# Performance work log

Measured on AMD Instinct MI355X. Metric: run time of the kernel, lower is better.

## Reference

```python
import jax, jax.numpy as jnp
import numpy as np
from jax import lax

H = 64          # lstm_units per direction
FEAT = 128      # input feature dim
EMB = 128       # dense output dim (embedding_dim)
B, T = 512, 512


def setup_inputs() -> dict:
    key = jax.random.key(0)
    ks = jax.random.split(key, 9)
    s = 0.05
    return {
        "x": jax.random.normal(ks[0], (B, T, FEAT), dtype=jnp.float32),
        # Keras LSTM kernels: input kernel [F, 4H], recurrent kernel [H, 4H], bias [4H]
        # gate order: i, f, g(cell), o
        "W_fwd": jax.random.normal(ks[1], (FEAT, 4 * H), dtype=jnp.float32) * s,
        "U_fwd": jax.random.normal(ks[2], (H, 4 * H), dtype=jnp.float32) * s,
        "b_fwd": jnp.zeros((4 * H,), dtype=jnp.float32),
        "W_bwd": jax.random.normal(ks[3], (FEAT, 4 * H), dtype=jnp.float32) * s,
        "U_bwd": jax.random.normal(ks[4], (H, 4 * H), dtype=jnp.float32) * s,
        "b_bwd": jnp.zeros((4 * H,), dtype=jnp.float32),
        "W_dense": jax.random.normal(ks[5], (2 * H, EMB), dtype=jnp.float32) * s,
        "b_dense": jnp.zeros((EMB,), dtype=jnp.float32),
    }


def _lstm_last(x, W, U, b):
    """Run an LSTM over x [B,T,F]; return last hidden state [B,H]."""
    bsz = x.shape[0]
    # precompute input projections for all timesteps (one big GEMM)
    xp = jnp.einsum('btf,fg->btg', x, W) + b      # [B,T,4H]
    xp = jnp.swapaxes(xp, 0, 1)                   # [T,B,4H]
    h0 = jnp.zeros((bsz, H), x.dtype)
    c0 = jnp.zeros((bsz, H), x.dtype)

    def step(carry, xt):
        h, c = carry
        z = xt + h @ U                            # [B,4H]
        i = jax.nn.sigmoid(z[:, :H])
        f = jax.nn.sigmoid(z[:, H:2 * H])
        g = jnp.tanh(z[:, 2 * H:3 * H])
        o = jax.nn.sigmoid(z[:, 3 * H:])
        c = f * c + i * g
        h = o * jnp.tanh(c)
        return (h, c), None

    (h, _), _ = lax.scan(step, (h0, c0), xp)
    return h


def reference(x, W_fwd, U_fwd, b_fwd, W_bwd, U_bwd, b_bwd, W_dense, b_dense):
    # Bidirectional(LSTM(return_sequences=False)), merge_mode='concat'.
    # dropout=0.2 is inactive at inference (training=False), so no dropout here.
    h_f = _lstm_last(x, W_fwd, U_fwd, b_fwd)
    h_b = _lstm_last(x[:, ::-1, :], W_bwd, U_bwd, b_bwd)
    h = jnp.concatenate([h_f, h_b], axis=-1)      # [B, 2H]
    return jax.nn.relu(h @ W_dense + b_dense)     # [B, EMB]
```

## Files before the change

kernel.cpp:

```cpp
#include <hip/hip_runtime.h>
#include <hip/hip_bf16.h>

#define H 64
#define F 128
#define G4 256
#define T 512
#define B 512
#define RB 16
#define TC 8

typedef __attribute__((ext_vector_type(4))) float f32x4;
typedef __attribute__((ext_vector_type(8))) short bf16x8;

__device__ __forceinline__ short f2bf(float f) {
    union { float f; unsigned u; } v; v.f = f;
    unsigned r = (v.u + 0x7fffu + ((v.u >> 16) & 1u)) >> 16;
    return (short)r;
}
__device__ __forceinline__ short f2bf_cvt(float f) {
    unsigned r;
    asm("v_cvt_pk_bf16_f32 %0, %1, %1" : "=v"(r) : "v"(f));
    return (short)r;
}
__device__ __forceinline__ unsigned cvtpk(float lo, float hi) {
    unsigned r;
    asm("v_cvt_pk_bf16_f32 %0, %1, %2" : "=v"(r) : "v"(lo), "v"(hi));
    return r;
}
__device__ __forceinline__ float bf2f(short s) {
    union { unsigned u; float f; } v; v.u = ((unsigned)(unsigned short)s) << 16;
    return v.f;
}
__device__ __forceinline__ float bflo(unsigned u) {
    union { unsigned u; float f; } v; v.u = u << 16; return v.f;
}
__device__ __forceinline__ float bfhi(unsigned u) {
    union { unsigned u; float f; } v; v.u = u & 0xffff0000u; return v.f;
}
__device__ __forceinline__ float sigf(float x) {
    return __builtin_amdgcn_rcpf(1.f + __expf(-x));
}
__device__ __forceinline__ float tanhf_(float x) {
    float e = __expf(2.f * x);
    return 1.f - 2.f * __builtin_amdgcn_rcpf(e + 1.f);
}

#define LOADX(XR, TT) do {                                                     \
    int _b = (TT) * F + 4 * lq;                                                \
    _Pragma("unroll")                                                          \
    for (int kt = 0; kt < 4; ++kt) {                                           \
        XR[kt][0] = *(const f32x4*)(xlane + _b + 32 * kt);                     \
        XR[kt][1] = *(const f32x4*)(xlane + _b + 32 * kt + 16);                \
    }                                                                          \
} while (0)

#define STOREXP(DIRBASE, SLOT, ACC) do {                                       \
    size_t _base = ((size_t)((DIRBASE) + rowg * 4 + lq) * (T / 2)              \
                    + ((SLOT) >> 1)) * 4096                                    \
                   + ((SLOT) & 1) * 512 + (16 * w + lr) * 8;                   \
    _Pragma("unroll")                                                          \
    for (int e = 0; e < 4; ++e) {                                              \
        uint2 pv;                                                              \
        pv.x = cvtpk(ACC[0][e], ACC[1][e]);                                    \
        pv.y = cvtpk(ACC[2][e], ACC[3][e]);                                    \
        *(uint2*)(xpb + _base + e * 1024) = pv;                                \
    }                                                                          \
} while (0)

#define XBODY2(TCUR, XR) do {                                                  \
    bf16x8 af[4];                                                              \
    _Pragma("unroll")                                                          \
    for (int kt = 0; kt < 4; ++kt) {                                           \
        bf16x8 v;                                                              \
        _Pragma("unroll")                                                      \
        for (int e = 0; e < 4; ++e) {                                          \
            v[e]     = f2bf(XR[kt][0][e]);                                     \
            v[e + 4] = f2bf(XR[kt][1][e]);                                     \
        }                                                                      \
        af[kt] = v;                                                            \
    }                                                                          \
    {   int tn = (TCUR) + 2; if (tn > T - 1) tn = T - 1;                       \
        LOADX(XR, tn); }                                                       \
    {   f32x4 accf[4];                                                         \
        _Pragma("unroll")                                                      \
        for (int s = 0; s < 4; ++s)                                            \
            accf[s] = (f32x4){bscf[s], bscf[s], bscf[s], bscf[s]};             \
        _Pragma("unroll")                                                      \
        for (int kt = 0; kt < 4; ++kt)                                         \
            _Pragma("unroll")                                                  \
            for (int s = 0; s < 4; ++s)                                        \
                accf[s] = __builtin_amdgcn_mfma_f32_16x16x32_bf16(             \
                    af[kt], wff[kt][s], accf[s], 0, 0, 0);                     \
        STOREXP(0, (TCUR), accf);                                              \
    }                                                                          \
    {   f32x4 accb[4];                                                         \
        _Pragma("unroll")                                                      \
        for (int s = 0; s < 4; ++s)                                            \
            accb[s] = (f32x4){bscb[s], bscb[s], bscb[s], bscb[s]};             \
        _Pragma("unroll")                                                      \
        for (int kt = 0; kt < 4; ++kt)                                         \
            _Pragma("unroll")                                                  \
            for (int s = 0; s < 4; ++s)                                        \
                accb[s] = __builtin_amdgcn_mfma_f32_16x16x32_bf16(             \
                    af[kt], wfb[kt][s], accb[s], 0, 0, 0);                     \
        STOREXP(128, T - 1 - (TCUR), accb);                                    \
    }                                                                          \
} while (0)

__global__ __launch_bounds__(256, 1)
void xw_gemm(const float* __restrict__ x,
             const float* __restrict__ Wf, const float* __restrict__ bfv,
             const float* __restrict__ Wb, const float* __restrict__ bbv,
             char* __restrict__ xpb) {
    const int tid = threadIdx.x;
    const int l = tid & 63, w = tid >> 6;
    const int lq = l >> 4, lr = l & 15;
    const int rowg = blockIdx.x >> 3;
    const int tc   = blockIdx.x & 7;
    const int r0 = rowg * RB;
    const int t0 = tc * (T / TC);

    bf16x8 wff[4][4], wfb[4][4];
#pragma unroll
    for (int kt = 0; kt < 4; ++kt)
#pragma unroll
        for (int s = 0; s < 4; ++s) {
            int col = (w + 4 * s) * 16 + lr;
            int k0 = kt * 32 + 4 * lq;
            bf16x8 vf, vb;
#pragma unroll
            for (int e = 0; e < 4; ++e) {
                vf[e]     = f2bf(Wf[(k0 + e) * G4 + col]);
                vf[e + 4] = f2bf(Wf[(k0 + 16 + e) * G4 + col]);
                vb[e]     = f2bf(Wb[(k0 + e) * G4 + col]);
                vb[e + 4] = f2bf(Wb[(k0 + 16 + e) * G4 + col]);
            }
            wff[kt][s] = vf;
            wfb[kt][s] = vb;
        }
    float bscf[4], bscb[4];
#pragma unroll
    for (int s = 0; s < 4; ++s) {
        bscf[s] = bfv[(w + 4 * s) * 16 + lr];
        bscb[s] = bbv[(w + 4 * s) * 16 + lr];
    }

    const float* xlane = x + (size_t)(r0 + lr) * (T * F);

    f32x4 xrA[4][2], xrB[4][2];
    LOADX(xrA, t0);
    LOADX(xrB, t0 + 1);

    for (int t = t0; t < t0 + T / TC; t += 2) {
        XBODY2(t,     xrA);
        XBODY2(t + 1, xrB);
    }
}

#define STAGE(PAIR, BUF) do {                                                  \
    int _p = (PAIR); if (_p > T / 2 - 1) _p = T / 2 - 1;                       \
    const char* _g = (const char*)xpc + ((size_t)_p * 4 + w) * 1024 + 16 * l;  \
    char* _lb = xps + (BUF) * 4096 + w * 1024;                                 \
    __builtin_amdgcn_global_load_lds(                                          \
        (const __attribute__((address_space(1))) void*)_g,                     \
        (__attribute__((address_space(3))) void*)_lb, 16, 0, 0);               \
} while (0)

#define RSTEP(TCUR, BUF, PRD, PWR, DOSTAGE) do {                               \
    bf16x8 hf0 = *(const bf16x8*)(hlds + (PRD) * 2048 + rd_off);               \
    bf16x8 hf1 = *(const bf16x8*)(hlds + (PRD) * 2048 + 1024 + rd_off);        \
    f32x4 acc[4];                                                              \
    _Pragma("unroll")                                                          \
    for (int s = 0; s < 4; ++s) acc[s] = (f32x4){0.f, 0.f, 0.f, 0.f};          \
    _Pragma("unroll")                                                          \
    for (int s = 0; s < 4; ++s)                                                \
        acc[s] = __builtin_amdgcn_mfma_f32_16x16x32_bf16(                      \
            hf0, ufr[0][s], acc[s], 0, 0, 0);                                  \
    _Pragma("unroll")                                                          \
    for (int s = 0; s < 4; ++s)                                                \
        acc[s] = __builtin_amdgcn_mfma_f32_16x16x32_bf16(                      \
            hf1, ufr[1][s], acc[s], 0, 0, 0);                                  \
    if (lq == 0) {                                                             \
        _Pragma("unroll")                                                      \
        for (int e = 0; e < 4; ++e) {                                          \
            f32x4 zw = {acc[0][e], acc[1][e], acc[2][e], acc[3][e]};           \
            *(f32x4*)(zbc + e * 1024 + w * 256 + lr * 16) = zw;                \
        }                                                                      \
    }                                                                          \
    asm volatile("s_waitcnt lgkmcnt(0)" ::: "memory");                         \
    __builtin_amdgcn_s_barrier();                                              \
    asm volatile("s_waitcnt vmcnt(3)" ::: "memory");                           \
    __builtin_amdgcn_sched_barrier(0);                                         \
    f32x4 zv = *(const f32x4*)(zbc + tid * 16);                                \
    uint2 xv = *(const uint2*)(xps + (BUF) * 4096 + w * 1024                   \
                               + ((TCUR) & 1) * 512 + l * 8);                  \
    float zi = zv[0] + bflo(xv.x);                                             \
    float zf = zv[1] + bfhi(xv.x);                                             \
    float zg = zv[2] + bflo(xv.y);                                             \
    float zo = zv[3] + bfhi(xv.y);                                             \
    float ei = __expf(-zi);                                                    \
    float ef = __expf(-zf);                                                    \
    float eg = __expf(2.f * fminf(zg, 15.f));                                  \
    float sf = __builtin_amdgcn_rcpf(1.f + ef);                                \
    float dig = __builtin_amdgcn_rcpf((1.f + ei) * (1.f + eg));                \
    cc = fmaf(sf, cc, (eg - 1.f) * dig);                                       \
    float eo = __expf(-zo);                                                    \
    float ec = __expf(2.f * fminf(cc, 15.f));                                  \
    float doc = __builtin_amdgcn_rcpf((1.f + eo) * (1.f + ec));                \
    hh = (ec - 1.f) * doc;                                                     \
    *(short*)(hlds + (PWR) * 2048 + wr) = f2bf_cvt(hh);                        \
    asm volatile("s_waitcnt lgkmcnt(0)" ::: "memory");                         \
    if (DOSTAGE) { STAGE(((TCUR) >> 1) + 4, BUF); }                            \
    __builtin_amdgcn_sched_barrier(0);                                         \
    __builtin_amdgcn_s_barrier();                                              \
    __builtin_amdgcn_sched_barrier(0);                                         \
} while (0)

__global__ __launch_bounds__(256, 1)
void lstm_rec(const char* __restrict__ xpb,
              const float* __restrict__ Uf, const float* __restrict__ Ub,
              float* __restrict__ hcat ) {
    const int tid = threadIdx.x;
    const int l = tid & 63, w = tid >> 6;
    const int lq = l >> 4, lr = l & 15;
    const int dir = blockIdx.x >> 7;
    const int rowg = blockIdx.x & 127;
    const int r0 = rowg * 4;

    const float* __restrict__ Um = dir ? Ub : Uf;

    bf16x8 ufr[2][4];
#pragma unroll
    for (int kt = 0; kt < 2; ++kt)
#pragma unroll
        for (int s = 0; s < 4; ++s) {
            int col = (w + 4 * s) * 16 + lr;
            int k0 = kt * 32 + 4 * lq;
            bf16x8 v;
#pragma unroll
            for (int e = 0; e < 4; ++e) {
                v[e]     = f2bf(Um[(k0 + e) * G4 + col]);
                v[e + 4] = f2bf(Um[(k0 + 16 + e) * G4 + col]);
            }
            ufr[kt][s] = v;
        }

    __shared__ __align__(16) char xps[4 * 4096];
    __shared__ __align__(16) char hlds[4096];
    __shared__ __align__(16) char zbc[4096];

    ((f32x4*)hlds)[tid] = (f32x4){0.f, 0.f, 0.f, 0.f};
    __syncthreads();

    const int rd_off = (l * 16) ^ (((l >> 4) & 3) << 4);

    const int gj = l;
    int wr;
    {
        int fl = w + 16 * ((gj >> 2) & 3);
        wr = (gj >> 5) * 1024 + ((fl * 16) ^ (((fl >> 4) & 3) << 4))
             + ((gj & 3) + 4 * ((gj >> 4) & 1)) * 2;
    }

    const char* xpc = xpb + (size_t)(dir * 128 + rowg) * (T / 2) * 4096;

    STAGE(0, 0);
    STAGE(1, 1);
    STAGE(2, 2);
    STAGE(3, 3);

    float cc = 0.f, hh = 0.f;

    for (int t = 0; t < T; t += 8) {
        RSTEP(t + 0, 0, 0, 1, 0);
        RSTEP(t + 1, 0, 1, 0, 1);
        RSTEP(t + 2, 1, 0, 1, 0);
        RSTEP(t + 3, 1, 1, 0, 1);
        RSTEP(t + 4, 2, 0, 1, 0);
        RSTEP(t + 5, 2, 1, 0, 1);
        RSTEP(t + 6, 3, 0, 1, 0);
        RSTEP(t + 7, 3, 1, 0, 1);
    }

    hcat[(size_t)(r0 + w) * (2 * H) + dir * H + l] = hh;
}

#define BODY(TCUR, XR, PRD, PWR) do {                                          \
    bf16x8 af[4];                                                              \
    _Pragma("unroll")                                                          \
    for (int kt = 0; kt < 4; ++kt) {                                           \
        bf16x8 v;                                                              \
        _Pragma("unroll")                                                      \
        for (int e = 0; e < 4; ++e) {                                          \
            v[e]     = f2bf(XR[kt][0][e]);                                     \
            v[e + 4] = f2bf(XR[kt][1][e]);                                     \
        }                                                                      \
        af[kt] = v;                                                            \
    }                                                                          \
    {   int tn = (TCUR) + 2; if (tn > T - 1) tn = T - 1;                       \
        int ttn = dir ? (T - 1 - tn) : tn;                                     \
        LOADX(XR, ttn); }                                                      \
    bf16x8 hf0 = *(const bf16x8*)(hlds + (PRD) * 2048 + rd_off);               \
    bf16x8 hf1 = *(const bf16x8*)(hlds + (PRD) * 2048 + 1024 + rd_off);        \
    f32x4 acc[4];                                                              \
    _Pragma("unroll")                                                          \
    for (int s = 0; s < 4; ++s)                                                \
        acc[s] = (f32x4){bsc[s], bsc[s], bsc[s], bsc[s]};                      \
    _Pragma("unroll")                                                          \
    for (int kt = 0; kt < 4; ++kt)                                             \
        _Pragma("unroll")                                                      \
        for (int s = 0; s < 4; ++s)                                            \
            acc[s] = __builtin_amdgcn_mfma_f32_16x16x32_bf16(                  \
                af[kt], wfr[kt][s], acc[s], 0, 0, 0);                          \
    _Pragma("unroll")                                                          \
    for (int s = 0; s < 4; ++s)                                                \
        acc[s] = __builtin_amdgcn_mfma_f32_16x16x32_bf16(                      \
            hf0, ufr[0][s], acc[s], 0, 0, 0);                                  \
    _Pragma("unroll")                                                          \
    for (int s = 0; s < 4; ++s)                                                \
        acc[s] = __builtin_amdgcn_mfma_f32_16x16x32_bf16(                      \
            hf1, ufr[1][s], acc[s], 0, 0, 0);                                  \
    _Pragma("unroll")                                                          \
    for (int e = 0; e < 4; ++e) {                                              \
        float ig = sigf(acc[0][e]);                                            \
        float fg = sigf(acc[1][e]);                                            \
        float gg = tanhf_(acc[2][e]);                                          \
        float og = sigf(acc[3][e]);                                            \
        c4[e] = fmaf(fg, c4[e], ig * gg);                                      \
        hq[e] = og * tanhf_(c4[e]);                                            \
        *(short*)(hlds + (PWR) * 2048 + wr_off[e]) = f2bf(hq[e]);              \
    }                                                                          \
    __syncthreads();                                                           \
} while (0)

__global__ __launch_bounds__(256, 1)
void lstm_mfma(const float* __restrict__ x,
               const float* __restrict__ Wf, const float* __restrict__ Uf,
               const float* __restrict__ bfv,
               const float* __restrict__ Wb, const float* __restrict__ Ub,
               const float* __restrict__ bbv,
               float* __restrict__ hcat) {
    const int tid = threadIdx.x;
    const int l = tid & 63, w = tid >> 6;
    const int lq = l >> 4, lr = l & 15;
    const int dir = blockIdx.x >> 5;
    const int r0 = (blockIdx.x & 31) * RB;

    const float* __restrict__ Wm = dir ? Wb : Wf;
    const float* __restrict__ Um = dir ? Ub : Uf;
    const float* __restrict__ bv = dir ? bbv : bfv;

    bf16x8 wfr[4][4];
#pragma unroll
    for (int kt = 0; kt < 4; ++kt)
#pragma unroll
        for (int s = 0; s < 4; ++s) {
            int col = (w + 4 * s) * 16 + lr;
            int k0 = kt * 32 + 4 * lq;
            bf16x8 v;
#pragma unroll
            for (int e = 0; e < 4; ++e) {
                v[e]     = f2bf(Wm[(k0 + e) * G4 + col]);
                v[e + 4] = f2bf(Wm[(k0 + 16 + e) * G4 + col]);
            }
            wfr[kt][s] = v;
        }
    bf16x8 ufr[2][4];
#pragma unroll
    for (int kt = 0; kt < 2; ++kt)
#pragma unroll
        for (int s = 0; s < 4; ++s) {
            int col = (w + 4 * s) * 16 + lr;
            int k0 = kt * 32 + 4 * lq;
            bf16x8 v;
#pragma unroll
            for (int e = 0; e < 4; ++e) {
                v[e]     = f2bf(Um[(k0 + e) * G4 + col]);
                v[e + 4] = f2bf(Um[(k0 + 16 + e) * G4 + col]);
            }
            ufr[kt][s] = v;
        }
    float bsc[4];
#pragma unroll
    for (int s = 0; s < 4; ++s) bsc[s] = bv[(w + 4 * s) * 16 + lr];

    __shared__ __align__(16) char hlds[4096];
    ((f32x4*)hlds)[tid] = (f32x4){0.f, 0.f, 0.f, 0.f};
    __syncthreads();

    const int rd_off = (l * 16) ^ (((l >> 4) & 3) << 4);
    const int j = 16 * w + lr;
    const int kt_j = j >> 5;
    const int elem_j = (j & 3) + 4 * ((j >> 4) & 1);
    int wr_off[4];
#pragma unroll
    for (int e = 0; e < 4; ++e) {
        int fl = 4 * lq + e + 16 * ((j >> 2) & 3);
        wr_off[e] = kt_j * 1024 + ((fl * 16) ^ (((fl >> 4) & 3) << 4)) + elem_j * 2;
    }

    const float* xlane = x + (size_t)(r0 + lr) * (T * F);

    f32x4 xrA[4][2], xrB[4][2];
    { int tt0 = dir ? (T - 1) : 0; LOADX(xrA, tt0); }
    { int tt1 = dir ? (T - 2) : 1; LOADX(xrB, tt1); }

    float c4[4] = {0.f, 0.f, 0.f, 0.f};
    float hq[4] = {0.f, 0.f, 0.f, 0.f};

    for (int t = 0; t < T; t += 2) {
        BODY(t,     xrA, 0, 1);
        BODY(t + 1, xrB, 1, 0);
    }

#pragma unroll
    for (int e = 0; e < 4; ++e) {
        int row = 4 * lq + e;
        hcat[(size_t)(r0 + row) * (2 * H) + dir * H + j] = hq[e];
    }
}

__global__ void dense_kernel(const float* __restrict__ hcat,
                             const float* __restrict__ Wd,
                             const float* __restrict__ bd,
                             float* __restrict__ out) {
    const int b = blockIdx.x;
    const int e = threadIdx.x;
    float acc = bd[e];
#pragma unroll
    for (int k = 0; k < 2 * H; ++k)
        acc = fmaf(hcat[b * (2 * H) + k], Wd[k * 128 + e], acc);
    out[b * 128 + e] = fmaxf(acc, 0.f);
}

extern "C" void kernel_launch(void* const* d_in, const int* in_sizes, int n_in,
                              void* d_out, int out_size, void* d_ws, size_t ws_size,
                              hipStream_t stream) {
    const float* x       = (const float*)d_in[0];
    const float* W_fwd   = (const float*)d_in[1];
    const float* U_fwd   = (const float*)d_in[2];
    const float* b_fwd   = (const float*)d_in[3];
    const float* W_bwd   = (const float*)d_in[4];
    const float* U_bwd   = (const float*)d_in[5];
    const float* b_bwd   = (const float*)d_in[6];
    const float* W_dense = (const float*)d_in[7];
    const float* b_dense = (const float*)d_in[8];
    float* out = (float*)d_out;

    const size_t XP_BYTES = (size_t)256 * (T / 2) * 4096;
    const size_t HCAT_BYTES = (size_t)B * 2 * H * 4;

    if (ws_size >= XP_BYTES + HCAT_BYTES) {
        char*  xpb  = (char*)d_ws;
        float* hcat = (float*)((char*)d_ws + XP_BYTES);

        xw_gemm<<<dim3(32 * TC), dim3(256), 0, stream>>>(
            x, W_fwd, b_fwd, W_bwd, b_bwd, xpb);
        lstm_rec<<<dim3(256), dim3(256), 0, stream>>>(
            xpb, U_fwd, U_bwd, hcat);
        dense_kernel<<<dim3(B), dim3(128), 0, stream>>>(hcat, W_dense, b_dense, out);
    } else {
        float* hcat = (float*)d_ws;
        lstm_mfma<<<dim3(2 * (B / RB)), dim3(256), 0, stream>>>(
            x, W_fwd, U_fwd, b_fwd, W_bwd, U_bwd, b_bwd, hcat);
        dense_kernel<<<dim3(B), dim3(128), 0, stream>>>(hcat, W_dense, b_dense, out);
    }
}
```

Before: 319.4 us.

## Compute LSTM gates directly from MFMA accumulators, removing z-broadcast LDS round-trip and barrier

Instead of having lane quarter 0 write MFMA results to an LDS buffer, barrier, and have every thread read back one gate quadruple, the lq==0 lanes now compute all four rows' gate nonlinearities directly from their accumulators. The precomputed x-projection layout is changed so each such lane reads its 4 rows' gate inputs as two 16-byte loads, and the final hidden-state writes follow the new ownership. This drops one barrier and an LDS write/read per timestep on the serial recurrence path. In exchange only a quarter of the lanes do the transcendental work, four times serially, which lengthens the per-step dependent math.

Measured after the change: 410.2 us. +28.5%, slower.

```diff
diff --git a/kernel.cpp b/kernel.cpp
--- a/kernel.cpp
+++ b/kernel.cpp
@@ -57,14 +57,14 @@
 #define STOREXP(DIRBASE, SLOT, ACC) do {                                       \
     size_t _base = ((size_t)((DIRBASE) + rowg * 4 + lq) * (T / 2)              \
                     + ((SLOT) >> 1)) * 4096                                    \
-                   + ((SLOT) & 1) * 512 + (16 * w + lr) * 8;                   \
-    _Pragma("unroll")                                                          \
-    for (int e = 0; e < 4; ++e) {                                              \
-        uint2 pv;                                                              \
-        pv.x = cvtpk(ACC[0][e], ACC[1][e]);                                    \
-        pv.y = cvtpk(ACC[2][e], ACC[3][e]);                                    \
-        *(uint2*)(xpb + _base + e * 1024) = pv;                                \
-    }                                                                          \
+                   + w * 1024 + ((SLOT) & 1) * 512 + lr * 32;                  \
+    uint4 p0, p1;                                                              \
+    p0.x = cvtpk(ACC[0][0], ACC[1][0]); p0.y = cvtpk(ACC[2][0], ACC[3][0]);    \
+    p0.z = cvtpk(ACC[0][1], ACC[1][1]); p0.w = cvtpk(ACC[2][1], ACC[3][1]);    \
+    p1.x = cvtpk(ACC[0][2], ACC[1][2]); p1.y = cvtpk(ACC[2][2], ACC[3][2]);    \
+    p1.z = cvtpk(ACC[0][3], ACC[1][3]); p1.w = cvtpk(ACC[2][3], ACC[3][3]);    \
+    *(uint4*)(xpb + _base) = p0;                                               \
+    *(uint4*)(xpb + _base + 16) = p1;                                          \
 } while (0)
 
 #define XBODY2(TCUR, XR) do {                                                  \
@@ -180,35 +180,34 @@
     for (int s = 0; s < 4; ++s)                                                \
         acc[s] = __builtin_amdgcn_mfma_f32_16x16x32_bf16(                      \
             hf1, ufr[1][s], acc[s], 0, 0, 0);                                  \
-    if (lq == 0) {                                                             \
-        _Pragma("unroll")                                                      \
-        for (int e = 0; e < 4; ++e) {                                          \
-            f32x4 zw = {acc[0][e], acc[1][e], acc[2][e], acc[3][e]};           \
-            *(f32x4*)(zbc + e * 1024 + w * 256 + lr * 16) = zw;                \
-        }                                                                      \
-    }                                                                          \
-    asm volatile("s_waitcnt lgkmcnt(0)" ::: "memory");                         \
-    __builtin_amdgcn_s_barrier();                                              \
     asm volatile("s_waitcnt vmcnt(3)" ::: "memory");                           \
     __builtin_amdgcn_sched_barrier(0);                                         \
-    f32x4 zv = *(const f32x4*)(zbc + tid * 16);                                \
-    uint2 xv = *(const uint2*)(xps + (BUF) * 4096 + w * 1024                   \
-                               + ((TCUR) & 1) * 512 + l * 8);                  \
-    float zi = zv[0] + bflo(xv.x);                                             \
-    float zf = zv[1] + bfhi(xv.x);                                             \
-    float zg = zv[2] + bflo(xv.y);                                             \
-    float zo = zv[3] + bfhi(xv.y);                                             \
-    float ei = __expf(-zi);                                                    \
-    float ef = __expf(-zf);                                                    \
-    float eg = __expf(2.f * fminf(zg, 15.f));                                  \
-    float sf = __builtin_amdgcn_rcpf(1.f + ef);                                \
-    float dig = __builtin_amdgcn_rcpf((1.f + ei) * (1.f + eg));                \
-    cc = fmaf(sf, cc, (eg - 1.f) * dig);                                       \
-    float eo = __expf(-zo);                                                    \
-    float ec = __expf(2.f * fminf(cc, 15.f));                                  \
-    float doc = __builtin_amdgcn_rcpf((1.f + eo) * (1.f + ec));                \
-    hh = (ec - 1.f) * doc;                                                     \
-    *(short*)(hlds + (PWR) * 2048 + wr) = f2bf_cvt(hh);                        \
+    if (lq == 0) {                                                             \
+        const char* _xb = xps + (BUF) * 4096 + w * 1024                        \
+                          + ((TCUR) & 1) * 512 + lr * 32;                      \
+        uint4 xv0 = *(const uint4*)_xb;                                        \
+        uint4 xv1 = *(const uint4*)(_xb + 16);                                 \
+        unsigned xg[8] = {xv0.x, xv0.y, xv0.z, xv0.w,                          \
+                          xv1.x, xv1.y, xv1.z, xv1.w};                         \
+        _Pragma("unroll")                                                      \
+        for (int e = 0; e < 4; ++e) {                                          \
+            float zi = acc[0][e] + bflo(xg[2 * e]);                            \
+            float zf = acc[1][e] + bfhi(xg[2 * e]);                            \
+            float zg = acc[2][e] + bflo(xg[2 * e + 1]);                        \
+            float zo = acc[3][e] + bfhi(xg[2 * e + 1]);                        \
+            float ei = __expf(-zi);                                            \
+            float ef = __expf(-zf);                                            \
+            float eg = __expf(2.f * fminf(zg, 15.f));                          \
+            float sf = __builtin_amdgcn_rcpf(1.f + ef);                        \
+            float dig = __builtin_amdgcn_rcpf((1.f + ei) * (1.f + eg));        \
+            cc[e] = fmaf(sf, cc[e], (eg - 1.f) * dig);                         \
+            float eo = __expf(-zo);                                            \
+            float ec = __expf(2.f * fminf(cc[e], 15.f));                       \
+            float doc = __builtin_amdgcn_rcpf((1.f + eo) * (1.f + ec));        \
+            hh[e] = (ec - 1.f) * doc;                                          \
+            *(short*)(hlds + (PWR) * 2048 + wr_off[e]) = f2bf_cvt(hh[e]);      \
+        }                                                                      \
+    }                                                                          \
     asm volatile("s_waitcnt lgkmcnt(0)" ::: "memory");                         \
     if (DOSTAGE) { STAGE(((TCUR) >> 1) + 4, BUF); }                            \
     __builtin_amdgcn_sched_barrier(0);                                         \
@@ -247,19 +246,22 @@
 
     __shared__ __align__(16) char xps[4 * 4096];
     __shared__ __align__(16) char hlds[4096];
-    __shared__ __align__(16) char zbc[4096];
-
-    ((f32x4*)hlds)[tid] = (f32x4){0.f, 0.f, 0.f, 0.f};
+
+    ((f32x4*)hlds)[tid & 255] = (f32x4){0.f, 0.f, 0.f, 0.f};
     __syncthreads();
 
     const int rd_off = (l * 16) ^ (((l >> 4) & 3) << 4);
 
-    const int gj = l;
-    int wr;
+    int wr_off[4];
     {
-        int fl = w + 16 * ((gj >> 2) & 3);
-        wr = (gj >> 5) * 1024 + ((fl * 16) ^ (((fl >> 4) & 3) << 4))
-             + ((gj & 3) + 4 * ((gj >> 4) & 1)) * 2;
+        int j = 16 * w + lr;
+        int elem_j = (j & 3) + 4 * ((j >> 4) & 1);
+#pragma unroll
+        for (int e = 0; e < 4; ++e) {
+            int fl = e + 16 * ((j >> 2) & 3);
+            wr_off[e] = (j >> 5) * 1024 + ((fl * 16) ^ (((fl >> 4) & 3) << 4))
+                        + elem_j * 2;
+        }
     }
 
     const char* xpc = xpb + (size_t)(dir * 128 + rowg) * (T / 2) * 4096;
@@ -269,7 +271,8 @@
     STAGE(2, 2);
     STAGE(3, 3);
 
-    float cc = 0.f, hh = 0.f;
+    float cc[4] = {0.f, 0.f, 0.f, 0.f};
+    float hh[4] = {0.f, 0.f, 0.f, 0.f};
 
     for (int t = 0; t < T; t += 8) {
         RSTEP(t + 0, 0, 0, 1, 0);
@@ -282,7 +285,11 @@
         RSTEP(t + 7, 3, 1, 0, 1);
     }
 
-    hcat[(size_t)(r0 + w) * (2 * H) + dir * H + l] = hh;
+    if (lq == 0) {
+#pragma unroll
+        for (int e = 0; e < 4; ++e)
+            hcat[(size_t)(r0 + e) * (2 * H) + dir * H + 16 * w + lr] = hh[e];
+    }
 }
 
 #define BODY(TCUR, XR, PRD, PWR) do {                                          \
```

## Halve rows per recurrent block to double grid and re-layout staged projections

Applied to the files above, without the earlier changes.

The recurrent kernel now handles 2 batch rows per block instead of 4, launching 512 blocks rather than 256. The precomputed input projections are re-laid out in quad-timestep chunks so that each 4 KB stage covers 4 timesteps for 2 rows. Only half of each wave's lanes run the gate math. This spreads the serial recurrence over more CUs to shorten the critical path. In exchange each MFMA does half-empty work, and one of the per-step barriers is removed.

New measurement: 340.5 us. +6.6%, slower.

```diff
diff --git a/kernel.cpp b/kernel.cpp
--- a/kernel.cpp
+++ b/kernel.cpp
@@ -55,15 +55,17 @@
 } while (0)
 
 #define STOREXP(DIRBASE, SLOT, ACC) do {                                       \
-    size_t _base = ((size_t)((DIRBASE) + rowg * 4 + lq) * (T / 2)              \
-                    + ((SLOT) >> 1)) * 4096                                    \
-                   + ((SLOT) & 1) * 512 + (16 * w + lr) * 8;                   \
     _Pragma("unroll")                                                          \
     for (int e = 0; e < 4; ++e) {                                              \
+        int grow = 4 * lq + e;                                                 \
+        size_t _a = ((size_t)((DIRBASE) + rowg * 8 + (grow >> 1)) * (T / 4)    \
+                     + ((SLOT) >> 2)) * 4096                                   \
+                    + w * 1024 + ((SLOT) & 3) * 256 + (grow & 1) * 128         \
+                    + lr * 8;                                                  \
         uint2 pv;                                                              \
         pv.x = cvtpk(ACC[0][e], ACC[1][e]);                                    \
         pv.y = cvtpk(ACC[2][e], ACC[3][e]);                                    \
-        *(uint2*)(xpb + _base + e * 1024) = pv;                                \
+        *(uint2*)(xpb + _a) = pv;                                              \
     }                                                                          \
 } while (0)
 
@@ -103,7 +105,7 @@
             for (int s = 0; s < 4; ++s)                                        \
                 accb[s] = __builtin_amdgcn_mfma_f32_16x16x32_bf16(             \
                     af[kt], wfb[kt][s], accb[s], 0, 0, 0);                     \
-        STOREXP(128, T - 1 - (TCUR), accb);                                    \
+        STOREXP(256, T - 1 - (TCUR), accb);                                    \
     }                                                                          \
 } while (0)
 
@@ -157,9 +159,9 @@
     }
 }
 
-#define STAGE(PAIR, BUF) do {                                                  \
-    int _p = (PAIR); if (_p > T / 2 - 1) _p = T / 2 - 1;                       \
-    const char* _g = (const char*)xpc + ((size_t)_p * 4 + w) * 1024 + 16 * l;  \
+#define STAGE(QUAD, BUF) do {                                                  \
+    int _q = (QUAD); if (_q > T / 4 - 1) _q = T / 4 - 1;                       \
+    const char* _g = (const char*)xpc + (size_t)_q * 4096 + w * 1024 + 16 * l; \
     char* _lb = xps + (BUF) * 4096 + w * 1024;                                 \
     __builtin_amdgcn_global_load_lds(                                          \
         (const __attribute__((address_space(1))) void*)_g,                     \
@@ -182,35 +184,37 @@
             hf1, ufr[1][s], acc[s], 0, 0, 0);                                  \
     if (lq == 0) {                                                             \
         _Pragma("unroll")                                                      \
-        for (int e = 0; e < 4; ++e) {                                          \
+        for (int e = 0; e < 2; ++e) {                                          \
             f32x4 zw = {acc[0][e], acc[1][e], acc[2][e], acc[3][e]};           \
             *(f32x4*)(zbc + e * 1024 + w * 256 + lr * 16) = zw;                \
         }                                                                      \
     }                                                                          \
     asm volatile("s_waitcnt lgkmcnt(0)" ::: "memory");                         \
-    __builtin_amdgcn_s_barrier();                                              \
     asm volatile("s_waitcnt vmcnt(3)" ::: "memory");                           \
     __builtin_amdgcn_sched_barrier(0);                                         \
-    f32x4 zv = *(const f32x4*)(zbc + tid * 16);                                \
-    uint2 xv = *(const uint2*)(xps + (BUF) * 4096 + w * 1024                   \
-                               + ((TCUR) & 1) * 512 + l * 8);                  \
-    float zi = zv[0] + bflo(xv.x);                                             \
-    float zf = zv[1] + bfhi(xv.x);                                             \
-    float zg = zv[2] + bflo(xv.y);                                             \
-    float zo = zv[3] + bfhi(xv.y);                                             \
-    float ei = __expf(-zi);                                                    \
-    float ef = __expf(-zf);                                                    \
-    float eg = __expf(2.f * fminf(zg, 15.f));                                  \
-    float sf = __builtin_amdgcn_rcpf(1.f + ef);                                \
-    float dig = __builtin_amdgcn_rcpf((1.f + ei) * (1.f + eg));                \
-    cc = fmaf(sf, cc, (eg - 1.f) * dig);                                       \
-    float eo = __expf(-zo);                                                    \
-    float ec = __expf(2.f * fminf(cc, 15.f));                                  \
-    float doc = __builtin_amdgcn_rcpf((1.f + eo) * (1.f + ec));                \
-    hh = (ec - 1.f) * doc;                                                     \
-    *(short*)(hlds + (PWR) * 2048 + wr) = f2bf_cvt(hh);                        \
+    if (l < 32) {                                                              \
+        int row = l >> 4, ju = l & 15;                                         \
+        f32x4 zv = *(const f32x4*)(zbc + row * 1024 + w * 256 + ju * 16);      \
+        uint2 xv = *(const uint2*)(xps + (BUF) * 4096 + w * 1024               \
+                                   + ((TCUR) & 3) * 256 + row * 128 + ju * 8); \
+        float zi = zv[0] + bflo(xv.x);                                         \
+        float zf = zv[1] + bfhi(xv.x);                                         \
+        float zg = zv[2] + bflo(xv.y);                                         \
+        float zo = zv[3] + bfhi(xv.y);                                         \
+        float ei = __expf(-zi);                                                \
+        float ef = __expf(-zf);                                                \
+        float eg = __expf(2.f * fminf(zg, 15.f));                              \
+        float sf = __builtin_amdgcn_rcpf(1.f + ef);                            \
+        float dig = __builtin_amdgcn_rcpf((1.f + ei) * (1.f + eg));            \
+        cc = fmaf(sf, cc, (eg - 1.f) * dig);                                   \
+        float eo = __expf(-zo);                                                \
+        float ec = __expf(2.f * fminf(cc, 15.f));                              \
+        float doc = __builtin_amdgcn_rcpf((1.f + eo) * (1.f + ec));            \
+        hh = (ec - 1.f) * doc;                                                 \
+        *(short*)(hlds + (PWR) * 2048 + wr) = f2bf_cvt(hh);                    \
+    }                                                                          \
     asm volatile("s_waitcnt lgkmcnt(0)" ::: "memory");                         \
-    if (DOSTAGE) { STAGE(((TCUR) >> 1) + 4, BUF); }                            \
+    if (DOSTAGE) { STAGE(((TCUR) >> 2) + 4, BUF); }                            \
     __builtin_amdgcn_sched_barrier(0);                                         \
     __builtin_amdgcn_s_barrier();                                              \
     __builtin_amdgcn_sched_barrier(0);                                         \
@@ -223,9 +227,9 @@
     const int tid = threadIdx.x;
     const int l = tid & 63, w = tid >> 6;
     const int lq = l >> 4, lr = l & 15;
-    const int dir = blockIdx.x >> 7;
-    const int rowg = blockIdx.x & 127;
-    const int r0 = rowg * 4;
+    const int dir = blockIdx.x >> 8;
+    const int rowg = blockIdx.x & 255;
+    const int r0 = rowg * 2;
 
     const float* __restrict__ Um = dir ? Ub : Uf;
 
@@ -247,22 +251,23 @@
 
     __shared__ __align__(16) char xps[4 * 4096];
     __shared__ __align__(16) char hlds[4096];
-    __shared__ __align__(16) char zbc[4096];
+    __shared__ __align__(16) char zbc[2048];
 
     ((f32x4*)hlds)[tid] = (f32x4){0.f, 0.f, 0.f, 0.f};
     __syncthreads();
 
     const int rd_off = (l * 16) ^ (((l >> 4) & 3) << 4);
 
-    const int gj = l;
     int wr;
     {
-        int fl = w + 16 * ((gj >> 2) & 3);
-        wr = (gj >> 5) * 1024 + ((fl * 16) ^ (((fl >> 4) & 3) << 4))
-             + ((gj & 3) + 4 * ((gj >> 4) & 1)) * 2;
-    }
-
-    const char* xpc = xpb + (size_t)(dir * 128 + rowg) * (T / 2) * 4096;
+        int j = 16 * w + (l & 15);
+        int row = (l >> 4) & 1;
+        int fl = row + 16 * ((j >> 2) & 3);
+        wr = (j >> 5) * 1024 + ((fl * 16) ^ (((fl >> 4) & 3) << 4))
+             + ((j & 3) + 4 * ((j >> 4) & 1)) * 2;
+    }
+
+    const char* xpc = xpb + (size_t)(dir * 256 + rowg) * (T / 4) * 4096;
 
     STAGE(0, 0);
     STAGE(1, 1);
@@ -271,18 +276,27 @@
 
     float cc = 0.f, hh = 0.f;
 
-    for (int t = 0; t < T; t += 8) {
-        RSTEP(t + 0, 0, 0, 1, 0);
-        RSTEP(t + 1, 0, 1, 0, 1);
-        RSTEP(t + 2, 1, 0, 1, 0);
-        RSTEP(t + 3, 1, 1, 0, 1);
-        RSTEP(t + 4, 2, 0, 1, 0);
-        RSTEP(t + 5, 2, 1, 0, 1);
-        RSTEP(t + 6, 3, 0, 1, 0);
-        RSTEP(t + 7, 3, 1, 0, 1);
-    }
-
-    hcat[(size_t)(r0 + w) * (2 * H) + dir * H + l] = hh;
+    for (int t = 0; t < T; t += 16) {
+        RSTEP(t + 0,  0, 0, 1, 0);
+        RSTEP(t + 1,  0, 1, 0, 0);
+        RSTEP(t + 2,  0, 0, 1, 0);
+        RSTEP(t + 3,  0, 1, 0, 1);
+        RSTEP(t + 4,  1, 0, 1, 0);
+        RSTEP(t + 5,  1, 1, 0, 0);
+        RSTEP(t + 6,  1, 0, 1, 0);
+        RSTEP(t + 7,  1, 1, 0, 1);
+        RSTEP(t + 8,  2, 0, 1, 0);
+        RSTEP(t + 9,  2, 1, 0, 0);
+        RSTEP(t + 10, 2, 0, 1, 0);
+        RSTEP(t + 11, 2, 1, 0, 1);
+        RSTEP(t + 12, 3, 0, 1, 0);
+        RSTEP(t + 13, 3, 1, 0, 0);
+        RSTEP(t + 14, 3, 0, 1, 0);
+        RSTEP(t + 15, 3, 1, 0, 1);
+    }
+
+    if (l < 32)
+        hcat[(size_t)(r0 + (l >> 4)) * (2 * H) + dir * H + 16 * w + (l & 15)] = hh;
 }
 
 #define BODY(TCUR, XR, PRD, PWR) do {                                          \
@@ -447,7 +461,7 @@
     const float* b_dense = (const float*)d_in[8];
     float* out = (float*)d_out;
 
-    const size_t XP_BYTES = (size_t)256 * (T / 2) * 4096;
+    const size_t XP_BYTES = (size_t)512 * (T / 4) * 4096;
     const size_t HCAT_BYTES = (size_t)B * 2 * H * 4;
 
     if (ws_size >= XP_BYTES + HCAT_BYTES) {
@@ -456,7 +470,7 @@
 
         xw_gemm<<<dim3(32 * TC), dim3(256), 0, stream>>>(
             x, W_fwd, b_fwd, W_bwd, b_bwd, xpb);
-        lstm_rec<<<dim3(256), dim3(256), 0, stream>>>(
+        lstm_rec<<<dim3(512), dim3(256), 0, stream>>>(
             xpb, U_fwd, U_bwd, hcat);
         dense_kernel<<<dim3(B), dim3(128), 0, stream>>>(hcat, W_dense, b_dense, out);
     } else {
```
